# Performance work log

Measured on AMD Instinct MI355X. Metric: run time of the kernel, lower is better.

Reference implementation:

```python
import jax, jax.numpy as jnp
import numpy as np

D = 1024
H = 16
DH = D // H
FF = 4096
EPS = 1e-6


def setup_inputs() -> dict:
    key = jax.random.key(0)
    ks = jax.random.split(key, 8)
    s = 1.0 / np.sqrt(D)
    return {
        "x": jax.random.normal(ks[0], (2, 2048, D), jnp.float32),
        # attention projections stored [in, out] (math equals torch Linear x @ W.T)
        "w_q": jax.random.normal(ks[1], (D, D), jnp.float32) * s,
        "w_k": jax.random.normal(ks[2], (D, D), jnp.float32) * s,
        "w_v": jax.random.normal(ks[3], (D, D), jnp.float32) * s,
        "w_o": jax.random.normal(ks[4], (D, D), jnp.float32) * s,
        "w1": jax.random.normal(ks[5], (D, FF), jnp.float32) * s,
        "b1": jnp.zeros((FF,), jnp.float32),
        "w2": jax.random.normal(ks[6], (FF, D), jnp.float32) * (1.0 / np.sqrt(FF)),
        "b2": jnp.zeros((D,), jnp.float32),
        "g1": jnp.ones((D,), jnp.float32),
        "be1": jnp.zeros((D,), jnp.float32),
        "g2": jnp.ones((D,), jnp.float32),
        "be2": jnp.zeros((D,), jnp.float32),
    }


def _layernorm(x, gamma, beta):
    # torch .std() uses Bessel correction (ddof=1); note std+eps, not var+eps
    mean = jnp.mean(x, axis=-1, keepdims=True)
    std = jnp.std(x, axis=-1, keepdims=True, ddof=1)
    return gamma * (x - mean) / (std + EPS) + beta


def _attention(h, w_q, w_k, w_v, w_o):
    B, S, _ = h.shape
    q = (h @ w_q).reshape(B, S, H, DH)
    k = (h @ w_k).reshape(B, S, H, DH)
    v = (h @ w_v).reshape(B, S, H, DH)
    scores = jnp.einsum('bqhd,bkhd->bhqk', q, k) / np.sqrt(DH)  # [B,H,S,S]
    attn = jax.nn.softmax(scores, axis=-1)
    out = jnp.einsum('bhqk,bkhd->bqhd', attn, v).reshape(B, S, D)
    return out @ w_o


def reference(x, w_q, w_k, w_v, w_o, w1, b1, w2, b2, g1, be1, g2, be2):
    # pre-norm residual 1: self-attention (dropout=0 / eval)
    x = x + _attention(_layernorm(x, g1, be1), w_q, w_k, w_v, w_o)
    # pre-norm residual 2: FFN
    h = _layernorm(x, g2, be2)
    x = x + (jax.nn.relu(h @ w1 + b1) @ w2 + b2)
    return x
```

## Files before the change

kernel.cpp:

```cpp
#include <hip/hip_runtime.h>


typedef _Float16 half8 __attribute__((ext_vector_type(8)));
typedef _Float16 half4 __attribute__((ext_vector_type(4)));
typedef __fp16 fp16x2 __attribute__((ext_vector_type(2)));
typedef float floatx4 __attribute__((ext_vector_type(4)));

#define MAX3(a, b, c) fmaxf(fmaxf((a), (b)), (c))

__device__ __forceinline__ void async16(const void* g, void* l) {
    __builtin_amdgcn_global_load_lds((const __attribute__((address_space(1))) unsigned int*)g,
                                     (__attribute__((address_space(3))) unsigned int*)l,
                                     16, 0, 0);
}

__global__ __launch_bounds__(256) void ln_kernel(const float* __restrict__ x,
                                                 const float* __restrict__ g,
                                                 const float* __restrict__ be,
                                                 _Float16* __restrict__ out) {
    int row = blockIdx.x;
    int tid = threadIdx.x;
    floatx4 v = ((const floatx4*)(x + (size_t)row * 1024))[tid];
    float s = 0.f, ss = 0.f;
#pragma unroll
    for (int i = 0; i < 4; i++) { s += v[i]; ss += v[i] * v[i]; }
#pragma unroll
    for (int off = 1; off < 64; off <<= 1) {
        s += __shfl_xor(s, off);
        ss += __shfl_xor(ss, off);
    }
    __shared__ float sm[8];
    int wave = tid >> 6, lane = tid & 63;
    if (lane == 0) { sm[wave] = s; sm[wave + 4] = ss; }
    __syncthreads();
    s = sm[0] + sm[1] + sm[2] + sm[3];
    ss = sm[4] + sm[5] + sm[6] + sm[7];
    float mean = s * (1.f / 1024.f);
    float var = (ss - s * mean) * (1.f / 1023.f);
    float rs = 1.f / (sqrtf(fmaxf(var, 0.f)) + 1e-6f);
    floatx4 gv = ((const floatx4*)g)[tid];
    floatx4 bv = ((const floatx4*)be)[tid];
    half4 o;
#pragma unroll
    for (int i = 0; i < 4; i++) o[i] = (_Float16)(gv[i] * (v[i] - mean) * rs + bv[i]);
    ((half4*)(out + (size_t)row * 1024))[tid] = o;
}

__device__ __forceinline__ void convt_body(const float* __restrict__ W, int ldW,
                                           _Float16* __restrict__ WT, int Kr, float scale,
                                           int n0, int k0) {
    __shared__ float t[64][65];
    int tid = threadIdx.x;
    int r = tid >> 4, c4 = (tid & 15) * 4;
#pragma unroll
    for (int p = 0; p < 4; p++) {
        floatx4 v = *(const floatx4*)(W + (size_t)(k0 + r + p * 16) * ldW + n0 + c4);
#pragma unroll
        for (int j = 0; j < 4; j++) t[c4 + j][r + p * 16] = v[j];
    }
    __syncthreads();
#pragma unroll
    for (int p = 0; p < 4; p++) {
        int rr = r + p * 16;
        half4 o;
#pragma unroll
        for (int j = 0; j < 4; j++) o[j] = (_Float16)(t[rr][c4 + j] * scale);
        *(half4*)(WT + (size_t)(n0 + rr) * Kr + k0 + c4) = o;
    }
}

__global__ __launch_bounds__(256) void convt_kernel(const float* __restrict__ W, int ldW,
                                                    _Float16* __restrict__ WT, int Kr,
                                                    float scale) {
    convt_body(W, ldW, WT, Kr, scale, blockIdx.x * 64, blockIdx.y * 64);
}

__global__ __launch_bounds__(256) void convt3_kernel(const float* __restrict__ W0,
                                                     const float* __restrict__ W1,
                                                     const float* __restrict__ W2,
                                                     _Float16* __restrict__ QT) {
    int z = blockIdx.z;
    const float* W = (z == 0) ? W0 : (z == 1) ? W1 : W2;
    _Float16* WT = QT + (size_t)z * 1024 * 1024;
    float scale = (z == 0) ? 0.125f : 1.f;
    convt_body(W, 1024, WT, 1024, scale, blockIdx.x * 64, blockIdx.y * 64);
}

__global__ __launch_bounds__(256) void convt_pair_kernel(const float* __restrict__ Wa, int ldWa,
                                                         _Float16* __restrict__ WTa, int Kra,
                                                         int gxa, int gya,
                                                         const float* __restrict__ Wb, int ldWb,
                                                         _Float16* __restrict__ WTb, int Krb,
                                                         int gxb, int gyb) {
    int z = blockIdx.z;
    const float* W = z ? Wb : Wa;
    _Float16* WT = z ? WTb : WTa;
    int ldW = z ? ldWb : ldWa;
    int Kr = z ? Krb : Kra;
    int gx = z ? gxb : gxa, gy = z ? gyb : gya;
    if ((int)blockIdx.x >= gx || (int)blockIdx.y >= gy) return;
    convt_body(W, ldW, WT, Kr, 1.f, blockIdx.x * 64, blockIdx.y * 64);
}

__global__ __launch_bounds__(256) void gemm_t(const _Float16* __restrict__ A, int lda,
                                              const _Float16* __restrict__ BT,
                                              const float* __restrict__ bias,
                                              const float* res, void* Cout,
                                              int N, int K, int relu_flag, int out_fp16) {
    __shared__ _Float16 As[64 * 64];
    __shared__ _Float16 Bs[128 * 64];
    int tid = threadIdx.x;
    int wave = tid >> 6, lane = tid & 63, quad = lane >> 4, l15 = lane & 15;
    int bm = blockIdx.y * 64, bn = blockIdx.x * 128;
    int wr = (wave & 1) * 32, wc = (wave >> 1) * 64;
    int lrow = lane >> 3, lch = lane & 7;

    floatx4 acc[2][4];
#pragma unroll
    for (int im = 0; im < 2; im++)
#pragma unroll
        for (int in = 0; in < 4; in++)
#pragma unroll
            for (int r = 0; r < 4; r++) acc[im][in][r] = 0.f;

    for (int k0 = 0; k0 < K; k0 += 64) {
        __syncthreads();
#pragma unroll
        for (int ia = 0; ia < 2; ia++) {
            int g = 2 * wave + ia;
            int row = g * 8 + lrow;
            int ch = lch ^ (row & 7);
            async16(A + (size_t)(bm + row) * lda + k0 + ch * 8, &As[g * 512]);
        }
#pragma unroll
        for (int ib = 0; ib < 4; ib++) {
            int g = 4 * wave + ib;
            int row = g * 8 + lrow;
            int ch = lch ^ (row & 7);
            async16(BT + (size_t)(bn + row) * K + k0 + ch * 8, &Bs[g * 512]);
        }
        __syncthreads();

        half8 af[2][2], bf[4][2];
#pragma unroll
        for (int kk = 0; kk < 2; kk++) {
#pragma unroll
            for (int im = 0; im < 2; im++) {
                int m = wr + im * 16 + l15;
                af[im][kk] = *(const half8*)&As[m * 64 + ((((kk << 2) | quad) ^ (m & 7)) << 3)];
            }
#pragma unroll
            for (int in = 0; in < 4; in++) {
                int n = wc + in * 16 + l15;
                bf[in][kk] = *(const half8*)&Bs[n * 64 + ((((kk << 2) | quad) ^ (n & 7)) << 3)];
            }
        }
#pragma unroll
        for (int kk = 0; kk < 2; kk++)
#pragma unroll
            for (int im = 0; im < 2; im++)
#pragma unroll
                for (int in = 0; in < 4; in++)
                    acc[im][in] = __builtin_amdgcn_mfma_f32_16x16x32_f16(af[im][kk], bf[in][kk],
                                                                         acc[im][in], 0, 0, 0);
    }
#pragma unroll
    for (int im = 0; im < 2; im++)
#pragma unroll
        for (int in = 0; in < 4; in++)
#pragma unroll
            for (int r = 0; r < 4; r++) {
                int row = bm + wr + im * 16 + quad * 4 + r;
                int col = bn + wc + in * 16 + l15;
                float val = acc[im][in][r];
                if (bias) val += bias[col];
                if (relu_flag) val = fmaxf(val, 0.f);
                if (res) val += res[(size_t)row * N + col];
                if (out_fp16) ((_Float16*)Cout)[(size_t)row * N + col] = (_Float16)val;
                else          ((float*)Cout)[(size_t)row * N + col] = val;
            }
}

__global__ __launch_bounds__(256) void gemm_t128(const _Float16* __restrict__ A, int lda,
                                                 const _Float16* __restrict__ BT,
                                                 _Float16* __restrict__ Cout,
                                                 _Float16* __restrict__ VtOut,
                                                 int N, int K) {
    __shared__ _Float16 As[128 * 64];
    __shared__ _Float16 Bs[128 * 64];
    int tid = threadIdx.x;
    int wave = tid >> 6, lane = tid & 63, quad = lane >> 4, l15 = lane & 15;
    int bm = blockIdx.y * 128, bn = blockIdx.x * 128;
    int wr = (wave & 1) * 64, wc = (wave >> 1) * 64;
    int lrow = lane >> 3, lch = lane & 7;

    floatx4 acc[4][4];
#pragma unroll
    for (int im = 0; im < 4; im++)
#pragma unroll
        for (int in = 0; in < 4; in++)
#pragma unroll
            for (int r = 0; r < 4; r++) acc[im][in][r] = 0.f;

    for (int k0 = 0; k0 < K; k0 += 64) {
        __syncthreads();
#pragma unroll
        for (int ia = 0; ia < 4; ia++) {
            int g = 4 * wave + ia;
            int row = g * 8 + lrow;
            int ch = lch ^ (row & 7);
            async16(A + (size_t)(bm + row) * lda + k0 + ch * 8, &As[g * 512]);
        }
#pragma unroll
        for (int ib = 0; ib < 4; ib++) {
            int g = 4 * wave + ib;
            int row = g * 8 + lrow;
            int ch = lch ^ (row & 7);
            async16(BT + (size_t)(bn + row) * K + k0 + ch * 8, &Bs[g * 512]);
        }
        __syncthreads();

        half8 af[4][2], bf[4][2];
#pragma unroll
        for (int kk = 0; kk < 2; kk++) {
#pragma unroll
            for (int im = 0; im < 4; im++) {
                int m = wr + im * 16 + l15;
                af[im][kk] = *(const half8*)&As[m * 64 + ((((kk << 2) | quad) ^ (m & 7)) << 3)];
            }
#pragma unroll
            for (int in = 0; in < 4; in++) {
                int n = wc + in * 16 + l15;
                bf[in][kk] = *(const half8*)&Bs[n * 64 + ((((kk << 2) | quad) ^ (n & 7)) << 3)];
            }
        }
#pragma unroll
        for (int kk = 0; kk < 2; kk++)
#pragma unroll
            for (int im = 0; im < 4; im++)
#pragma unroll
                for (int in = 0; in < 4; in++)
                    acc[im][in] = __builtin_amdgcn_mfma_f32_16x16x32_f16(af[im][kk], bf[in][kk],
                                                                         acc[im][in], 0, 0, 0);
    }
    if (VtOut && bn >= 2048) {
#pragma unroll
        for (int im = 0; im < 4; im++) {
            int rowbase = bm + wr + im * 16 + quad * 4;
            int b = rowbase >> 11, s = rowbase & 2047;
#pragma unroll
            for (int in = 0; in < 4; in++) {
                int vcol = bn - 2048 + wc + in * 16 + l15;
                int bh = b * 16 + (vcol >> 6);
                int dh = vcol & 63;
                half4 o;
#pragma unroll
                for (int r = 0; r < 4; r++) o[r] = (_Float16)acc[im][in][r];
                *(half4*)&VtOut[((size_t)bh * 64 + dh) * 2048 + s] = o;
            }
        }
    } else {
#pragma unroll
        for (int im = 0; im < 4; im++)
#pragma unroll
            for (int in = 0; in < 4; in++)
#pragma unroll
                for (int r = 0; r < 4; r++) {
                    int row = bm + wr + im * 16 + quad * 4 + r;
                    int col = bn + wc + in * 16 + l15;
                    Cout[(size_t)row * N + col] = (_Float16)acc[im][in][r];
                }
    }
}

template <int BUF>
__device__ __forceinline__ void attn_step(const half8* const (&kfp)[2][4][2],
                                          const half4* const (&vfp)[2][4][4],
                                          const half8 (&bq)[2],
                                          floatx4 (&o_acc)[4],
                                          float& m_i, float& l_i) {
    const float LOG2E = 1.44269504f;
    floatx4 s_acc[4];
#pragma unroll
    for (int jn = 0; jn < 4; jn++)
#pragma unroll
        for (int r = 0; r < 4; r++) s_acc[jn][r] = 0.f;
#pragma unroll
    for (int jn = 0; jn < 4; jn++)
#pragma unroll
        for (int kk = 0; kk < 2; kk++)
            s_acc[jn] = __builtin_amdgcn_mfma_f32_16x16x32_f16(*kfp[BUF][jn][kk], bq[kk],
                                                               s_acc[jn], 0, 0, 0);

    float t0 = MAX3(s_acc[0][0], s_acc[0][1], s_acc[0][2]);
    float t1 = MAX3(s_acc[0][3], s_acc[1][0], s_acc[1][1]);
    float t2 = MAX3(s_acc[1][2], s_acc[1][3], s_acc[2][0]);
    float t3 = MAX3(s_acc[2][1], s_acc[2][2], s_acc[2][3]);
    float t4 = MAX3(s_acc[3][0], s_acc[3][1], s_acc[3][2]);
    float mx = MAX3(MAX3(t0, t1, t2), fmaxf(t3, t4), s_acc[3][3]);
    mx = fmaxf(mx, __shfl_xor(mx, 16));
    mx = fmaxf(mx, __shfl_xor(mx, 32));
    if (!__all(mx <= m_i + 8.f)) {
        float mnew = fmaxf(m_i, mx);
        float dd = m_i - mnew;
        float alpha = (dd < -60.f) ? 0.f : __expf(dd);
        l_i *= alpha;
#pragma unroll
        for (int im = 0; im < 4; im++)
#pragma unroll
            for (int r = 0; r < 4; r++) o_acc[im][r] *= alpha;
        m_i = mnew;
    }
    float m2 = m_i * LOG2E;

    float sj[4];
    half4 pb[4];
#pragma unroll
    for (int jn = 0; jn < 4; jn++) {
        float p0 = exp2f(fmaf(s_acc[jn][0], LOG2E, -m2));
        float p1 = exp2f(fmaf(s_acc[jn][1], LOG2E, -m2));
        float p2 = exp2f(fmaf(s_acc[jn][2], LOG2E, -m2));
        float p3 = exp2f(fmaf(s_acc[jn][3], LOG2E, -m2));
        sj[jn] = (p0 + p1) + (p2 + p3);
        fp16x2 lo = __builtin_amdgcn_cvt_pkrtz(p0, p1);
        fp16x2 hi = __builtin_amdgcn_cvt_pkrtz(p2, p3);
        pb[jn][0] = (_Float16)lo[0]; pb[jn][1] = (_Float16)lo[1];
        pb[jn][2] = (_Float16)hi[0]; pb[jn][3] = (_Float16)hi[1];
    }
    float sum = (sj[0] + sj[1]) + (sj[2] + sj[3]);
    sum += __shfl_xor(sum, 16);
    sum += __shfl_xor(sum, 32);
    l_i += sum;

#pragma unroll
    for (int im = 0; im < 4; im++)
#pragma unroll
        for (int ks = 0; ks < 4; ks++)
            o_acc[im] = __builtin_amdgcn_mfma_f32_16x16x16f16(*vfp[BUF][im][ks], pb[ks],
                                                              o_acc[im], 0, 0, 0);
}

__global__ __launch_bounds__(256) void attn_kernel(const _Float16* Q,
                                                   const _Float16* __restrict__ K,
                                                   const _Float16* __restrict__ Vt,
                                                   _Float16* O, int ld) {
    __shared__ _Float16 KVs[2][2][64 * 64];
    int qt = blockIdx.x, bh = blockIdx.y;
    int b = bh >> 4, h = bh & 15;
    int col0 = h * 64, tbase = b * 2048;
    int tid = threadIdx.x;
    int wave = tid >> 6, lane = tid & 63, quad = lane >> 4, l15 = lane & 15;
    int lrow = lane >> 3, lch = lane & 7;

    const _Float16* kg[2];
    const _Float16* vg[2];
    const size_t kadv = (size_t)64 * ld;
#pragma unroll
    for (int i = 0; i < 2; i++) {
        int g = 2 * wave + i;
        int row = g * 8 + lrow;
        int ch = lch ^ (row & 7);
        kg[i] = K + (size_t)(tbase + row) * ld + col0 + ch * 8;
        vg[i] = Vt + ((size_t)bh * 64 + row) * 2048 + ch * 8;
        async16(Q + (size_t)(tbase + qt * 64 + row) * ld + col0 + ch * 8, &KVs[1][0][g * 512]);
        async16(kg[i], &KVs[0][0][g * 512]);
        async16(vg[i], &KVs[0][1][g * 512]);
        kg[i] += kadv;
        vg[i] += 64;
    }
    __syncthreads();

    int rowq = 16 * wave + l15;
    half8 bq[2];
#pragma unroll
    for (int kk = 0; kk < 2; kk++)
        bq[kk] = *(const half8*)&KVs[1][0][rowq * 64 + ((((kk << 2) | quad) ^ (rowq & 7)) << 3)];
    asm volatile("s_waitcnt lgkmcnt(0)" ::: "memory");
    __builtin_amdgcn_sched_barrier(0);

    const half8* kfp[2][4][2];
    const half4* vfp[2][4][4];
#pragma unroll
    for (int bb = 0; bb < 2; bb++) {
#pragma unroll
        for (int jn = 0; jn < 4; jn++) {
            int rowk = 16 * jn + l15;
#pragma unroll
            for (int kk = 0; kk < 2; kk++)
                kfp[bb][jn][kk] = (const half8*)
                    &KVs[bb][0][rowk * 64 + ((((kk << 2) | quad) ^ (rowk & 7)) << 3)];
        }
#pragma unroll
        for (int im = 0; im < 4; im++) {
            int rowv = 16 * im + l15;
#pragma unroll
            for (int ks = 0; ks < 4; ks++) {
                int off = rowv * 128 + ((((2 * ks) | (quad >> 1)) ^ (rowv & 7)) << 4)
                          + (quad & 1) * 8;
                vfp[bb][im][ks] = (const half4*)((const char*)KVs[bb][1] + off);
            }
        }
    }

    floatx4 o_acc[4];
#pragma unroll
    for (int im = 0; im < 4; im++)
#pragma unroll
        for (int r = 0; r < 4; r++) o_acc[im][r] = 0.f;
    float m_i = -1e30f, l_i = 0.f;

#pragma unroll 1
    for (int kt2 = 0; kt2 < 16; kt2++) {
        if (kt2) __syncthreads();
#pragma unroll
        for (int i = 0; i < 2; i++) {
            async16(kg[i], &KVs[1][0][(2 * wave + i) * 512]);
            async16(vg[i], &KVs[1][1][(2 * wave + i) * 512]);
            kg[i] += kadv;
            vg[i] += 64;
        }
        attn_step<0>(kfp, vfp, bq, o_acc, m_i, l_i);

        __syncthreads();
        if (kt2 < 15) {
#pragma unroll
            for (int i = 0; i < 2; i++) {
                async16(kg[i], &KVs[0][0][(2 * wave + i) * 512]);
                async16(vg[i], &KVs[0][1][(2 * wave + i) * 512]);
                kg[i] += kadv;
                vg[i] += 64;
            }
        }
        attn_step<1>(kfp, vfp, bq, o_acc, m_i, l_i);
    }

    float rl = 1.f / l_i;
#pragma unroll
    for (int im = 0; im < 4; im++) {
        half4 o;
#pragma unroll
        for (int r = 0; r < 4; r++) o[r] = (_Float16)(o_acc[im][r] * rl);
        *(half4*)&O[(size_t)(tbase + qt * 64 + wave * 16 + l15) * ld + col0 + im * 16 + quad * 4] = o;
    }
}

extern "C" void kernel_launch(void* const* d_in, const int* in_sizes, int n_in,
                              void* d_out, int out_size, void* d_ws, size_t ws_size,
                              hipStream_t stream) {
    const float* x   = (const float*)d_in[0];
    const float* wq  = (const float*)d_in[1];
    const float* wk  = (const float*)d_in[2];
    const float* wv  = (const float*)d_in[3];
    const float* wo  = (const float*)d_in[4];
    const float* w1  = (const float*)d_in[5];
    const float* b1  = (const float*)d_in[6];
    const float* w2  = (const float*)d_in[7];
    const float* b2  = (const float*)d_in[8];
    const float* g1  = (const float*)d_in[9];
    const float* be1 = (const float*)d_in[10];
    const float* g2  = (const float*)d_in[11];
    const float* be2 = (const float*)d_in[12];

    const size_t M1 = (size_t)1 << 20;
    _Float16* R0  = (_Float16*)d_ws;
    _Float16* QKV = R0 + 4 * M1;
    _Float16* R3  = R0 + 12 * M1;

    _Float16* wqkvT = (_Float16*)d_out;
    _Float16* VtD = wqkvT + 3 * M1;
    float* x1 = (float*)d_out;
    float* out = (float*)d_out;

    dim3 blk(256);

    convt3_kernel<<<dim3(16, 16, 3), blk, 0, stream>>>(wq, wk, wv, wqkvT);
    ln_kernel<<<4096, blk, 0, stream>>>(x, g1, be1, R0);
    gemm_t128<<<dim3(24, 32), blk, 0, stream>>>(R0, 1024, wqkvT, QKV, VtD, 3072, 1024);
    attn_kernel<<<dim3(32, 32), blk, 0, stream>>>(QKV, QKV + 1024, VtD, QKV, 3072);
    _Float16* woT = R0;
    convt_kernel<<<dim3(16, 16), blk, 0, stream>>>(wo, 1024, woT, 1024, 1.f);
    gemm_t<<<dim3(8, 64), blk, 0, stream>>>(QKV, 3072, woT, nullptr, x, x1, 1024, 1024, 0, 0);
    ln_kernel<<<4096, blk, 0, stream>>>(x1, g2, be2, R0);
    _Float16* f = QKV;
    for (int hh = 0; hh < 2; hh++) {
        _Float16* w1Th = R3;
        _Float16* w2Th = R3 + 2 * M1;
        convt_pair_kernel<<<dim3(32, 32, 2), blk, 0, stream>>>(
            w1 + hh * 2048, 4096, w1Th, 1024, 32, 16,
            w2 + (size_t)hh * 2048 * 1024, 1024, w2Th, 2048, 16, 32);
        gemm_t<<<dim3(16, 64), blk, 0, stream>>>(R0, 1024, w1Th, b1 + hh * 2048, nullptr, f,
                                                 2048, 1024, 1, 1);
        gemm_t<<<dim3(8, 64), blk, 0, stream>>>(f, 2048, w2Th, (hh == 1) ? b2 : nullptr, x1, out,
                                                1024, 2048, 0, 0);
    }
}
```

Baseline: 421.2 us.

## Process two query tiles per attention block to reuse K/V tiles

Each attention workgroup now handles 128 query rows as two 64-row sub-tiles, with separate Q fragments, accumulators and softmax state. Every K/V tile loaded into shared memory is consumed twice, halving global and LDS traffic per query and the number of blocks launched. The cost is roughly double the accumulator register use, which may lower occupancy, and only 512 blocks to spread across the GPU.

```diff
diff --git a/kernel.cpp b/kernel.cpp
--- a/kernel.cpp
+++ b/kernel.cpp
@@ -274,11 +274,11 @@
 }
 
 template <int BUF>
-__device__ __forceinline__ void attn_step(const half8* const (&kfp)[2][4][2],
-                                          const half4* const (&vfp)[2][4][4],
-                                          const half8 (&bq)[2],
-                                          floatx4 (&o_acc)[4],
-                                          float& m_i, float& l_i) {
+__device__ __forceinline__ void attn_substep(const half8* const (&kfp)[2][4][2],
+                                             const half4* const (&vfp)[2][4][4],
+                                             const half8 (&bq)[2],
+                                             floatx4 (&o_acc)[4],
+                                             float& m_i, float& l_i) {
     const float LOG2E = 1.44269504f;
     floatx4 s_acc[4];
 #pragma unroll
@@ -362,7 +362,8 @@
         int ch = lch ^ (row & 7);
         kg[i] = K + (size_t)(tbase + row) * ld + col0 + ch * 8;
         vg[i] = Vt + ((size_t)bh * 64 + row) * 2048 + ch * 8;
-        async16(Q + (size_t)(tbase + qt * 64 + row) * ld + col0 + ch * 8, &KVs[1][0][g * 512]);
+        async16(Q + (size_t)(tbase + qt * 128 + row) * ld + col0 + ch * 8, &KVs[1][0][g * 512]);
+        async16(Q + (size_t)(tbase + qt * 128 + 64 + row) * ld + col0 + ch * 8, &KVs[1][1][g * 512]);
         async16(kg[i], &KVs[0][0][g * 512]);
         async16(vg[i], &KVs[0][1][g * 512]);
         kg[i] += kadv;
@@ -371,10 +372,13 @@
     __syncthreads();
 
     int rowq = 16 * wave + l15;
-    half8 bq[2];
-#pragma unroll
-    for (int kk = 0; kk < 2; kk++)
-        bq[kk] = *(const half8*)&KVs[1][0][rowq * 64 + ((((kk << 2) | quad) ^ (rowq & 7)) << 3)];
+    half8 bq0[2], bq1[2];
+#pragma unroll
+    for (int kk = 0; kk < 2; kk++) {
+        int off = rowq * 64 + ((((kk << 2) | quad) ^ (rowq & 7)) << 3);
+        bq0[kk] = *(const half8*)&KVs[1][0][off];
+        bq1[kk] = *(const half8*)&KVs[1][1][off];
+    }
     asm volatile("s_waitcnt lgkmcnt(0)" ::: "memory");
     __builtin_amdgcn_sched_barrier(0);
 
@@ -402,12 +406,12 @@
         }
     }
 
-    floatx4 o_acc[4];
+    floatx4 o_acc0[4], o_acc1[4];
 #pragma unroll
     for (int im = 0; im < 4; im++)
 #pragma unroll
-        for (int r = 0; r < 4; r++) o_acc[im][r] = 0.f;
-    float m_i = -1e30f, l_i = 0.f;
+        for (int r = 0; r < 4; r++) { o_acc0[im][r] = 0.f; o_acc1[im][r] = 0.f; }
+    float m0 = -1e30f, l0 = 0.f, m1 = -1e30f, l1 = 0.f;
 
 #pragma unroll 1
     for (int kt2 = 0; kt2 < 16; kt2++) {
@@ -419,7 +423,8 @@
             kg[i] += kadv;
             vg[i] += 64;
         }
-        attn_step<0>(kfp, vfp, bq, o_acc, m_i, l_i);
+        attn_substep<0>(kfp, vfp, bq0, o_acc0, m0, l0);
+        attn_substep<0>(kfp, vfp, bq1, o_acc1, m1, l1);
 
         __syncthreads();
         if (kt2 < 15) {
@@ -431,16 +436,20 @@
                 vg[i] += 64;
             }
         }
-        attn_step<1>(kfp, vfp, bq, o_acc, m_i, l_i);
-    }
-
-    float rl = 1.f / l_i;
+        attn_substep<1>(kfp, vfp, bq0, o_acc0, m0, l0);
+        attn_substep<1>(kfp, vfp, bq1, o_acc1, m1, l1);
+    }
+
+    float rl0 = 1.f / l0, rl1 = 1.f / l1;
 #pragma unroll
     for (int im = 0; im < 4; im++) {
         half4 o;
 #pragma unroll
-        for (int r = 0; r < 4; r++) o[r] = (_Float16)(o_acc[im][r] * rl);
-        *(half4*)&O[(size_t)(tbase + qt * 64 + wave * 16 + l15) * ld + col0 + im * 16 + quad * 4] = o;
+        for (int r = 0; r < 4; r++) o[r] = (_Float16)(o_acc0[im][r] * rl0);
+        *(half4*)&O[(size_t)(tbase + qt * 128 + wave * 16 + l15) * ld + col0 + im * 16 + quad * 4] = o;
+#pragma unroll
+        for (int r = 0; r < 4; r++) o[r] = (_Float16)(o_acc1[im][r] * rl1);
+        *(half4*)&O[(size_t)(tbase + qt * 128 + 64 + wave * 16 + l15) * ld + col0 + im * 16 + quad * 4] = o;
     }
 }
 
@@ -476,7 +485,7 @@
     convt3_kernel<<<dim3(16, 16, 3), blk, 0, stream>>>(wq, wk, wv, wqkvT);
     ln_kernel<<<4096, blk, 0, stream>>>(x, g1, be1, R0);
     gemm_t128<<<dim3(24, 32), blk, 0, stream>>>(R0, 1024, wqkvT, QKV, VtD, 3072, 1024);
-    attn_kernel<<<dim3(32, 32), blk, 0, stream>>>(QKV, QKV + 1024, VtD, QKV, 3072);
+    attn_kernel<<<dim3(16, 32), blk, 0, stream>>>(QKV, QKV + 1024, VtD, QKV, 3072);
     _Float16* woT = R0;
     convt_kernel<<<dim3(16, 16), blk, 0, stream>>>(wo, 1024, woT, 1024, 1.f);
     gemm_t<<<dim3(8, 64), blk, 0, stream>>>(QKV, 3072, woT, nullptr, x, x1, 1024, 1024, 0, 0);
```

After: 423.0 us. Within noise of the previous version (+0.4%).

## Triple-buffer K/V tiles in attention with vmcnt-based waits instead of full syncs

Applied to the files above, without the earlier changes.

Moves the attention kernel from double to triple buffering of K/V tiles in LDS. Each step waits with partial s_waitcnt vmcnt counts plus a barrier, so one tile stays in flight during compute instead of draining all loads with __syncthreads. The loop is unrolled by three buffers, with a two-step epilogue covering 32 tiles. LDS use grows from 32KB to 48KB per block, which may lower occupancy, and the hand-written vmcnt counts must stay correct.

```diff
diff --git a/kernel.cpp b/kernel.cpp
--- a/kernel.cpp
+++ b/kernel.cpp
@@ -274,8 +274,8 @@
 }
 
 template <int BUF>
-__device__ __forceinline__ void attn_step(const half8* const (&kfp)[2][4][2],
-                                          const half4* const (&vfp)[2][4][4],
+__device__ __forceinline__ void attn_step(const half8* const (&kfp)[3][4][2],
+                                          const half4* const (&vfp)[3][4][4],
                                           const half8 (&bq)[2],
                                           floatx4 (&o_acc)[4],
                                           float& m_i, float& l_i) {
@@ -344,7 +344,7 @@
                                                    const _Float16* __restrict__ K,
                                                    const _Float16* __restrict__ Vt,
                                                    _Float16* O, int ld) {
-    __shared__ _Float16 KVs[2][2][64 * 64];
+    __shared__ _Float16 KVs[3][2][64 * 64];
     int qt = blockIdx.x, bh = blockIdx.y;
     int b = bh >> 4, h = bh & 15;
     int col0 = h * 64, tbase = b * 2048;
@@ -355,6 +355,7 @@
     const _Float16* kg[2];
     const _Float16* vg[2];
     const size_t kadv = (size_t)64 * ld;
+
 #pragma unroll
     for (int i = 0; i < 2; i++) {
         int g = 2 * wave + i;
@@ -362,26 +363,34 @@
         int ch = lch ^ (row & 7);
         kg[i] = K + (size_t)(tbase + row) * ld + col0 + ch * 8;
         vg[i] = Vt + ((size_t)bh * 64 + row) * 2048 + ch * 8;
-        async16(Q + (size_t)(tbase + qt * 64 + row) * ld + col0 + ch * 8, &KVs[1][0][g * 512]);
+        async16(Q + (size_t)(tbase + qt * 64 + row) * ld + col0 + ch * 8, &KVs[2][0][g * 512]);
         async16(kg[i], &KVs[0][0][g * 512]);
         async16(vg[i], &KVs[0][1][g * 512]);
         kg[i] += kadv;
         vg[i] += 64;
     }
-    __syncthreads();
+#pragma unroll
+    for (int i = 0; i < 2; i++) {
+        async16(kg[i], &KVs[1][0][(2 * wave + i) * 512]);
+        async16(vg[i], &KVs[1][1][(2 * wave + i) * 512]);
+        kg[i] += kadv;
+        vg[i] += 64;
+    }
+    asm volatile("s_waitcnt vmcnt(6)" ::: "memory");
+    __builtin_amdgcn_sched_barrier(0);
 
     int rowq = 16 * wave + l15;
     half8 bq[2];
 #pragma unroll
     for (int kk = 0; kk < 2; kk++)
-        bq[kk] = *(const half8*)&KVs[1][0][rowq * 64 + ((((kk << 2) | quad) ^ (rowq & 7)) << 3)];
+        bq[kk] = *(const half8*)&KVs[2][0][rowq * 64 + ((((kk << 2) | quad) ^ (rowq & 7)) << 3)];
     asm volatile("s_waitcnt lgkmcnt(0)" ::: "memory");
     __builtin_amdgcn_sched_barrier(0);
 
-    const half8* kfp[2][4][2];
-    const half4* vfp[2][4][4];
-#pragma unroll
-    for (int bb = 0; bb < 2; bb++) {
+    const half8* kfp[3][4][2];
+    const half4* vfp[3][4][4];
+#pragma unroll
+    for (int bb = 0; bb < 3; bb++) {
 #pragma unroll
         for (int jn = 0; jn < 4; jn++) {
             int rowk = 16 * jn + l15;
@@ -409,30 +418,36 @@
         for (int r = 0; r < 4; r++) o_acc[im][r] = 0.f;
     float m_i = -1e30f, l_i = 0.f;
 
+#define ATTN_BODY(BUFI, STI)                                                       \
+    do {                                                                           \
+        asm volatile("s_waitcnt vmcnt(4)" ::: "memory");                           \
+        __builtin_amdgcn_s_barrier();                                              \
+        __builtin_amdgcn_sched_barrier(0);                                         \
+        _Pragma("unroll")                                                          \
+        for (int i = 0; i < 2; i++) {                                              \
+            async16(kg[i], &KVs[STI][0][(2 * wave + i) * 512]);                    \
+            async16(vg[i], &KVs[STI][1][(2 * wave + i) * 512]);                    \
+            kg[i] += kadv;                                                         \
+            vg[i] += 64;                                                           \
+        }                                                                          \
+        attn_step<BUFI>(kfp, vfp, bq, o_acc, m_i, l_i);                            \
+    } while (0)
+
 #pragma unroll 1
-    for (int kt2 = 0; kt2 < 16; kt2++) {
-        if (kt2) __syncthreads();
-#pragma unroll
-        for (int i = 0; i < 2; i++) {
-            async16(kg[i], &KVs[1][0][(2 * wave + i) * 512]);
-            async16(vg[i], &KVs[1][1][(2 * wave + i) * 512]);
-            kg[i] += kadv;
-            vg[i] += 64;
-        }
-        attn_step<0>(kfp, vfp, bq, o_acc, m_i, l_i);
-
-        __syncthreads();
-        if (kt2 < 15) {
-#pragma unroll
-            for (int i = 0; i < 2; i++) {
-                async16(kg[i], &KVs[0][0][(2 * wave + i) * 512]);
-                async16(vg[i], &KVs[0][1][(2 * wave + i) * 512]);
-                kg[i] += kadv;
-                vg[i] += 64;
-            }
-        }
-        attn_step<1>(kfp, vfp, bq, o_acc, m_i, l_i);
-    }
+    for (int t = 0; t < 10; t++) {
+        ATTN_BODY(0, 2);
+        ATTN_BODY(1, 0);
+        ATTN_BODY(2, 1);
+    }
+    asm volatile("s_waitcnt vmcnt(4)" ::: "memory");
+    __builtin_amdgcn_s_barrier();
+    __builtin_amdgcn_sched_barrier(0);
+    attn_step<0>(kfp, vfp, bq, o_acc, m_i, l_i);
+    asm volatile("s_waitcnt vmcnt(0)" ::: "memory");
+    __builtin_amdgcn_s_barrier();
+    __builtin_amdgcn_sched_barrier(0);
+    attn_step<1>(kfp, vfp, bq, o_acc, m_i, l_i);
+#undef ATTN_BODY
 
     float rl = 1.f / l_i;
 #pragma unroll
```

New measurement: 441.5 us. 4.8% more time.
